# Performance work log

Measured on AMD Instinct MI355X. Metric: run time of the kernel, lower is better.

Reference implementation:

```python
import jax, jax.numpy as jnp
import numpy as np

N_NODES = 100_000
N_EDGES = 3_200_000
F_IN = 64
HID = 16
N_CLASSES = 4


def setup_inputs() -> dict:
    key = jax.random.key(0)
    ks = jax.random.split(key, 9)
    x = jax.random.normal(ks[0], (N_NODES, F_IN), dtype=jnp.float32)
    edge_index = jax.random.randint(ks[1], (2, N_EDGES), 0, N_NODES, dtype=jnp.int64)
    edge_weight = jax.random.uniform(ks[2], (N_EDGES,), dtype=jnp.float32)
    # Glorot-style init for the three GCN layer weights, zero bias (PyG default)
    W1 = jax.random.normal(ks[3], (F_IN, HID), dtype=jnp.float32) * (1.0 / np.sqrt(F_IN))
    b1 = jnp.zeros((HID,), jnp.float32)
    W3 = jax.random.normal(ks[4], (HID, HID), dtype=jnp.float32) * (1.0 / np.sqrt(HID))
    b3 = jnp.zeros((HID,), jnp.float32)
    W2 = jax.random.normal(ks[5], (HID, N_CLASSES), dtype=jnp.float32) * (1.0 / np.sqrt(HID))
    b2 = jnp.zeros((N_CLASSES,), jnp.float32)
    return {"x": x, "edge_index": edge_index, "edge_weight": edge_weight,
            "W1": W1, "b1": b1, "W3": W3, "b3": b3, "W2": W2, "b2": b2}


def reference(x, edge_index, edge_weight, W1, b1, W3, b3, W2, b2):
    n = x.shape[0]
    # GCNConv default: add self-loops with weight 1, symmetric deg^-1/2 norm
    loop = jnp.arange(n, dtype=edge_index.dtype)
    row = jnp.concatenate([edge_index[0], loop])  # source nodes
    col = jnp.concatenate([edge_index[1], loop])  # target nodes
    ew = jnp.concatenate([edge_weight, jnp.ones((n,), edge_weight.dtype)])
    deg = jax.ops.segment_sum(ew, col, num_segments=n)
    dinv = jnp.where(deg > 0, jax.lax.rsqrt(deg), 0.0)
    norm = dinv[row] * ew * dinv[col]  # [E+N]

    def gcn_conv(h, W, b):
        h = h @ W                                  # [N, out] small matmul first
        msg = norm[:, None] * h[row]               # gather + scale, [E+N, out]
        return jax.ops.segment_sum(msg, col, num_segments=n) + b

    h = jax.nn.relu(gcn_conv(x, W1, b1))
    # dropout is identity in eval mode (training=False)
    h = jax.nn.relu(gcn_conv(h, W3, b3))
    h = gcn_conv(h, W2, b2)
    return jax.nn.log_softmax(h, axis=1)
```

## Files before the change

### kernel.cpp

```cpp
#include <hip/hip_runtime.h>
#include <math.h>

#define NN 100000
#define NE 3200000
#define F_IN 64
#define HID 16
#define NC 4

#define SZB 200
#define NB 500
#define CAP 7424
#define CH 8192
#define NCH 391
#define NW 16

typedef _Float16 half_t;
typedef _Float16 h4f __attribute__((ext_vector_type(4)));

__device__ __forceinline__ unsigned bdiv(unsigned c) {
    return (unsigned)(((unsigned long long)c * 167773ull) >> 25);
}

__device__ __forceinline__ float upw(int pk) {
    unsigned short us = (unsigned short)(pk & 0x7fff);
    half_t h;
    __builtin_memcpy(&h, &us, 2);
    return (float)h;
}

__global__ __launch_bounds__(1024) void k_bin(const int* __restrict__ row,
                                              const int* __restrict__ col,
                                              const float* __restrict__ ew,
                                              int* __restrict__ cursor,
                                              unsigned* __restrict__ bpk,
                                              unsigned char* __restrict__ bcl) {
    __shared__ int h[NB];
    __shared__ int lstart[NB];
    __shared__ int gbase[NB];
    __shared__ int wsum[16];
    __shared__ uint2 s2[CH];
    int tid = threadIdx.x;
    int lane = tid & 63, wv = tid >> 6;
    for (int i = tid; i < NB; i += 1024) h[i] = 0;
    __syncthreads();
    int e0 = blockIdx.x * CH;
    int e1 = min(e0 + CH, NE);
    int eCnt = e1 - e0;
    int4 c4s[2];
#pragma unroll
    for (int it = 0; it < 2; it++) {
        int i = e0 + tid * 4 + it * 4096;
        if (i < e1) {
            int4 c4 = *(const int4*)(col + i);
            c4s[it] = c4;
            atomicAdd(&h[bdiv(c4.x)], 1);
            atomicAdd(&h[bdiv(c4.y)], 1);
            atomicAdd(&h[bdiv(c4.z)], 1);
            atomicAdd(&h[bdiv(c4.w)], 1);
        }
    }
    __syncthreads();
    int c0 = (tid < NB) ? h[tid] : 0;
    int v = c0;
#pragma unroll
    for (int off = 1; off < 64; off <<= 1) {
        int t = __shfl_up(v, off, 64);
        if (lane >= off) v += t;
    }
    if (lane == 63) wsum[wv] = v;
    __syncthreads();
    if (tid < NB) {
        int pre = 0;
#pragma unroll
        for (int ww = 0; ww < 8; ww++) pre += (ww < wv) ? wsum[ww] : 0;
        int ex = (v + pre) - c0;
        lstart[tid] = ex;
        h[tid] = ex;
        if (c0) gbase[tid] = tid * CAP + atomicAdd(&cursor[tid], c0);
    }
    __syncthreads();
#pragma unroll
    for (int it = 0; it < 2; it++) {
        int i = e0 + tid * 4 + it * 4096;
        if (i < e1) {
            int4 c4 = c4s[it];
            int4 r4 = *(const int4*)(row + i);
            float4 w4 = *(const float4*)(ew + i);
            half_t hw0 = (half_t)w4.x, hw1 = (half_t)w4.y, hw2 = (half_t)w4.z, hw3 = (half_t)w4.w;
            unsigned short b0, b1, b2, b3;
            __builtin_memcpy(&b0, &hw0, 2); __builtin_memcpy(&b1, &hw1, 2);
            __builtin_memcpy(&b2, &hw2, 2); __builtin_memcpy(&b3, &hw3, 2);
            int p; unsigned bb;
            bb = bdiv(c4.x); p = atomicAdd(&h[bb], 1);
            s2[p] = make_uint2(((unsigned)r4.x << 15) | (b0 & 0x7fff),
                               (bb << 8) | (unsigned)(c4.x - 200u * bb));
            bb = bdiv(c4.y); p = atomicAdd(&h[bb], 1);
            s2[p] = make_uint2(((unsigned)r4.y << 15) | (b1 & 0x7fff),
                               (bb << 8) | (unsigned)(c4.y - 200u * bb));
            bb = bdiv(c4.z); p = atomicAdd(&h[bb], 1);
            s2[p] = make_uint2(((unsigned)r4.z << 15) | (b2 & 0x7fff),
                               (bb << 8) | (unsigned)(c4.z - 200u * bb));
            bb = bdiv(c4.w); p = atomicAdd(&h[bb], 1);
            s2[p] = make_uint2(((unsigned)r4.w << 15) | (b3 & 0x7fff),
                               (bb << 8) | (unsigned)(c4.w - 200u * bb));
        }
    }
    __syncthreads();
    for (int i = tid; i < eCnt; i += 1024) {
        uint2 e2 = s2[i];
        int lo = (int)(e2.y >> 8);
        int d = gbase[lo] + (i - lstart[lo]);
        if (d < (lo + 1) * CAP) {
            bpk[d] = e2.x;
            bcl[d] = (unsigned char)(e2.y & 255u);
        }
    }
}

__global__ __launch_bounds__(1024) void k_sort(const unsigned* __restrict__ bpk,
                                               const unsigned char* __restrict__ bcl,
                                               const int* __restrict__ cursor,
                                               const float* __restrict__ x,
                                               const float* __restrict__ W1,
                                               unsigned* __restrict__ epk,
                                               int2* __restrict__ nodeptr2,
                                               float* __restrict__ dinv,
                                               half_t* __restrict__ tt1,
                                               int* __restrict__ perm) {
    __shared__ int hw[NW][SZB];
    __shared__ int cnt[SZB];
    __shared__ int ps[SZB];
    __shared__ int wsum4[4];
    __shared__ int h2[64];
    __shared__ int h2b[64];
    __shared__ unsigned stage[CAP];
    __shared__ float Ws[F_IN * HID];
    int b = blockIdx.x, tid = threadIdx.x;
    int lane = tid & 63;
    int w = tid >> 6;
    for (int i = tid; i < NW * SZB; i += 1024) ((int*)hw)[i] = 0;
    for (int i = tid; i < F_IN * HID; i += 1024) Ws[i] = W1[i];
    if (tid < 64) h2[tid] = 0;
    __syncthreads();
    int s = b * CAP;
    int m = min(cursor[b], CAP);
    int e = s + m;
    for (int i = s + tid; i < e; i += 1024)
        atomicAdd(&hw[w][bcl[i]], 1);
    __syncthreads();
    if (tid < SZB) {
        int c = 0;
#pragma unroll
        for (int ww = 0; ww < NW; ww++) c += hw[ww][tid];
        cnt[tid] = c;
    }
    __syncthreads();
    int pc = (tid < SZB) ? ((cnt[tid] + 3) & ~3) : 0;
    int key = 0;
    if (tid < SZB) {
        key = min(pc >> 2, 63);
        atomicAdd(&h2[key], 1);
    }
    int v = pc;
#pragma unroll
    for (int off = 1; off < 64; off <<= 1) {
        int t = __shfl_up(v, off, 64);
        if (lane >= off) v += t;
    }
    if (w < 4 && lane == 63) wsum4[w] = v;
    __syncthreads();
    if (tid < SZB) {
        int pre = 0;
#pragma unroll
        for (int ww = 0; ww < 4; ww++) pre += (ww < w) ? wsum4[ww] : 0;
        ps[tid] = v + pre;
    }
    if (tid < 64) {
        int c2 = h2[tid];
        int v2 = c2;
#pragma unroll
        for (int off = 1; off < 64; off <<= 1) {
            int t = __shfl_up(v2, off, 64);
            if (lane >= off) v2 += t;
        }
        h2b[tid] = v2 - c2;
    }
    __syncthreads();
    if (tid < SZB) {
        int rk = atomicAdd(&h2b[key], 1);
        perm[b * SZB + rk] = b * SZB + tid;
    }
    if (tid < SZB) {
        int run = ps[tid] - pc;
#pragma unroll
        for (int ww = 0; ww < NW; ww++) {
            int t = hw[ww][tid];
            hw[ww][tid] = run;
            run += t;
        }
    }
    __syncthreads();
    int mpad = min(ps[SZB - 1], CAP);
    for (int i = tid; i < mpad; i += 1024) stage[i] = 0u;
    __syncthreads();
    for (int i = s + tid; i < e; i += 1024) {
        int cl = bcl[i];
        int pos = atomicAdd(&hw[w][cl], 1);
        if (pos < CAP) stage[pos] = bpk[i];
    }
    __syncthreads();
    for (int i = tid; i < mpad; i += 1024) epk[s + i] = stage[i];
    int nl = tid >> 2, l = tid & 3;
    float di = 0.0f;
    int n = b * SZB + nl;
    if (nl < SZB) {
        int pcn = (cnt[nl] + 3) & ~3;
        int ex = ps[nl] - pcn;
        float sw = 0.0f;
        for (int i = ex + l; i < ex + pcn; i += 4) sw += upw((int)stage[i]);
        sw += __shfl_xor(sw, 1, 4);
        sw += __shfl_xor(sw, 2, 4);
        di = rsqrtf(1.0f + sw);
        if (n < NN && l == 0) {
            nodeptr2[n] = make_int2(s + ex, s + ex + pcn);
            dinv[n] = di;
        }
    }
    if (nl < SZB && n < NN) {
        float part[HID];
#pragma unroll
        for (int j = 0; j < HID; j++) part[j] = 0.0f;
        const float4* xp = (const float4*)(x + (size_t)n * F_IN) + l * 4;
#pragma unroll
        for (int k4 = 0; k4 < 4; k4++) {
            float4 vx = xp[k4];
            int k = l * 16 + k4 * 4;
#pragma unroll
            for (int j = 0; j < HID; j++) {
                part[j] += vx.x * Ws[(k + 0) * HID + j];
                part[j] += vx.y * Ws[(k + 1) * HID + j];
                part[j] += vx.z * Ws[(k + 2) * HID + j];
                part[j] += vx.w * Ws[(k + 3) * HID + j];
            }
        }
#pragma unroll
        for (int j = 0; j < HID; j++) {
            part[j] += __shfl_xor(part[j], 1, 4);
            part[j] += __shfl_xor(part[j], 2, 4);
        }
        h4f o;
        o.x = (half_t)(di * part[4 * l + 0]);
        o.y = (half_t)(di * part[4 * l + 1]);
        o.z = (half_t)(di * part[4 * l + 2]);
        o.w = (half_t)(di * part[4 * l + 3]);
        ((h4f*)tt1)[n * 4 + l] = o;
    }
}

#define ACC4(Q, V0, V1, V2, V3)                                                 \
    do {                                                                        \
        float w0 = upw((Q).x), w1 = upw((Q).y), w2 = upw((Q).z), w3 = upw((Q).w); \
        ax += w0 * (float)(V0).x; ay += w0 * (float)(V0).y;                     \
        az += w0 * (float)(V0).z; aw += w0 * (float)(V0).w;                     \
        ax += w1 * (float)(V1).x; ay += w1 * (float)(V1).y;                     \
        az += w1 * (float)(V1).z; aw += w1 * (float)(V1).w;                     \
        ax += w2 * (float)(V2).x; ay += w2 * (float)(V2).y;                     \
        az += w2 * (float)(V2).z; aw += w2 * (float)(V2).w;                     \
        ax += w3 * (float)(V3).x; ay += w3 * (float)(V3).y;                     \
        az += w3 * (float)(V3).z; aw += w3 * (float)(V3).w;                     \
    } while (0)

template <int DN>
__global__ __launch_bounds__(256) void k_aggf(const unsigned* __restrict__ epk,
                                              const int2* __restrict__ nptr,
                                              const int* __restrict__ perm,
                                              const half_t* __restrict__ tt_in,
                                              const float* __restrict__ bias,
                                              const float* __restrict__ dinv,
                                              const float* __restrict__ Wn,
                                              half_t* __restrict__ tt_out) {
    __shared__ float Ws[HID * DN];
    if (threadIdx.x < HID * DN) Ws[threadIdx.x] = Wn[threadIdx.x];
    __syncthreads();
    int tid = blockIdx.x * 256 + threadIdx.x;
    int g = tid >> 2;
    int l = tid & 3;
    if (g >= NN) return;
    int n = perm[g];
    int2 p = nptr[n];
    const h4f* ttp = (const h4f*)tt_in;
    h4f sv = ttp[n * 4 + l];
    float ax = 0.f, ay = 0.f, az = 0.f, aw = 0.f;
    int base = p.x;
    const int pend = p.y;
    if (base < pend) {
        int4 q = *(const int4*)(epk + base);
        base += 4;
        bool more = base < pend;
        int4 qn = *(const int4*)(epk + (more ? base : p.x));
        h4f v0 = ttp[((((unsigned)q.x) >> 15) << 2) + l];
        h4f v1 = ttp[((((unsigned)q.y) >> 15) << 2) + l];
        h4f v2 = ttp[((((unsigned)q.z) >> 15) << 2) + l];
        h4f v3 = ttp[((((unsigned)q.w) >> 15) << 2) + l];
        while (more) {
            base += 4;
            bool more2 = base < pend;
            int4 qnn = *(const int4*)(epk + (more2 ? base : p.x));
            h4f u0 = ttp[((((unsigned)qn.x) >> 15) << 2) + l];
            h4f u1 = ttp[((((unsigned)qn.y) >> 15) << 2) + l];
            h4f u2 = ttp[((((unsigned)qn.z) >> 15) << 2) + l];
            h4f u3 = ttp[((((unsigned)qn.w) >> 15) << 2) + l];
            ACC4(q, v0, v1, v2, v3);
            q = qn; qn = qnn;
            v0 = u0; v1 = u1; v2 = u2; v3 = u3;
            more = more2;
        }
        ACC4(q, v0, v1, v2, v3);
    }
    float di = dinv[n];
    const float4* b4p = (const float4*)bias;
    float4 b4 = b4p[l];
    float hreg[4];
    hreg[0] = fmaxf(b4.x + di * (ax + (float)sv.x), 0.f);
    hreg[1] = fmaxf(b4.y + di * (ay + (float)sv.y), 0.f);
    hreg[2] = fmaxf(b4.z + di * (az + (float)sv.z), 0.f);
    hreg[3] = fmaxf(b4.w + di * (aw + (float)sv.w), 0.f);
    if (DN == 16) {
        float ox = 0.f, oy = 0.f, oz = 0.f, ow = 0.f;
#pragma unroll
        for (int k = 0; k < HID; k++) {
            float hk = __shfl(hreg[k & 3], k >> 2, 4);
            const float4 wk = *(const float4*)&Ws[k * 16 + 4 * l];
            ox += hk * wk.x; oy += hk * wk.y; oz += hk * wk.z; ow += hk * wk.w;
        }
        h4f ov;
        ov.x = (half_t)(di * ox); ov.y = (half_t)(di * oy);
        ov.z = (half_t)(di * oz); ov.w = (half_t)(di * ow);
        ((h4f*)tt_out)[n * 4 + l] = ov;
    } else {
        float o = 0.f;
#pragma unroll
        for (int k = 0; k < HID; k++) {
            float hk = __shfl(hreg[k & 3], k >> 2, 4);
            o += hk * Ws[k * DN + l];
        }
        tt_out[(size_t)n * DN + l] = (half_t)(di * o);
    }
}

__global__ __launch_bounds__(256) void k_agg4sm(const unsigned* __restrict__ epk,
                                                const int2* __restrict__ nptr,
                                                const int* __restrict__ perm,
                                                const half_t* __restrict__ tt,
                                                const float* __restrict__ bias,
                                                const float* __restrict__ dinv,
                                                float* __restrict__ out) {
    int tid = blockIdx.x * 256 + threadIdx.x;
    int g = tid >> 2;
    int l = tid & 3;
    if (g >= NN) return;
    int n = perm[g];
    int2 p = nptr[n];
    float self = (float)tt[n * 4 + l];
    float acc = 0.f;
    int base = p.x;
    const int pend = p.y;
    if (base < pend) {
        int4 q = *(const int4*)(epk + base);
        base += 4;
        bool more = base < pend;
        int4 qn = *(const int4*)(epk + (more ? base : p.x));
        float v0 = (float)tt[((((unsigned)q.x) >> 15) << 2) + l];
        float v1 = (float)tt[((((unsigned)q.y) >> 15) << 2) + l];
        float v2 = (float)tt[((((unsigned)q.z) >> 15) << 2) + l];
        float v3 = (float)tt[((((unsigned)q.w) >> 15) << 2) + l];
        while (more) {
            base += 4;
            bool more2 = base < pend;
            int4 qnn = *(const int4*)(epk + (more2 ? base : p.x));
            float u0 = (float)tt[((((unsigned)qn.x) >> 15) << 2) + l];
            float u1 = (float)tt[((((unsigned)qn.y) >> 15) << 2) + l];
            float u2 = (float)tt[((((unsigned)qn.z) >> 15) << 2) + l];
            float u3 = (float)tt[((((unsigned)qn.w) >> 15) << 2) + l];
            acc += upw(q.x) * v0;
            acc += upw(q.y) * v1;
            acc += upw(q.z) * v2;
            acc += upw(q.w) * v3;
            q = qn; qn = qnn;
            v0 = u0; v1 = u1; v2 = u2; v3 = u3;
            more = more2;
        }
        acc += upw(q.x) * v0;
        acc += upw(q.y) * v1;
        acc += upw(q.z) * v2;
        acc += upw(q.w) * v3;
    }
    float di = dinv[n];
    float logit = bias[l] + di * (acc + self);
    float mx = logit;
    mx = fmaxf(mx, __shfl_xor(mx, 1, 4));
    mx = fmaxf(mx, __shfl_xor(mx, 2, 4));
    float ex = expf(logit - mx);
    float sm = ex;
    sm += __shfl_xor(sm, 1, 4);
    sm += __shfl_xor(sm, 2, 4);
    out[n * 4 + l] = logit - mx - logf(sm);
}

extern "C" void kernel_launch(void* const* d_in, const int* in_sizes, int n_in,
                              void* d_out, int out_size, void* d_ws, size_t ws_size,
                              hipStream_t stream) {
    const float* x  = (const float*)d_in[0];
    const int*   ei = (const int*)d_in[1];
    const float* ew = (const float*)d_in[2];
    const float* W1 = (const float*)d_in[3];
    const float* b1 = (const float*)d_in[4];
    const float* W3 = (const float*)d_in[5];
    const float* b3 = (const float*)d_in[6];
    const float* W2 = (const float*)d_in[7];
    const float* b2 = (const float*)d_in[8];
    float* out = (float*)d_out;

    const int* row = ei;
    const int* col = ei + NE;

    const size_t NEP = (size_t)NB * CAP;
    char* ws = (char*)d_ws;
    size_t off = 0;
    float*         dinv     = (float*)(ws + off);         off += 400000;
    int2*          nodeptr2 = (int2*)(ws + off);          off += 800000;
    int*           cursor   = (int*)(ws + off);           off += 2048;
    int*           perm     = (int*)(ws + off);           off += 400000;
    unsigned*      epk      = (unsigned*)(ws + off);      off += NEP * 4;
    unsigned*      bpk      = (unsigned*)(ws + off);      off += NEP * 4;
    unsigned char* bcl      = (unsigned char*)(ws + off); off += (NEP + 15) & ~15ull;
    half_t*        tt1      = (half_t*)(ws + off);        off += (size_t)NN * HID * 2;
    half_t*        tt2      = (half_t*)(ws + off);        off += (size_t)NN * HID * 2;
    half_t*        tt3      = (half_t*)(ws + off);        off += (size_t)NN * NC * 2;

    hipMemsetAsync(cursor, 0, NB * sizeof(int), stream);

    k_bin<<<NCH, 1024, 0, stream>>>(row, col, ew, cursor, bpk, bcl);
    k_sort<<<NB, 1024, 0, stream>>>(bpk, bcl, cursor, x, W1, epk, nodeptr2, dinv, tt1, perm);

    int gA = (NN * 4 + 255) / 256;

    k_aggf<HID><<<gA, 256, 0, stream>>>(epk, nodeptr2, perm, tt1, b1, dinv, W3, tt2);
    k_aggf<NC><<<gA, 256, 0, stream>>>(epk, nodeptr2, perm, tt2, b3, dinv, W2, tt3);
    k_agg4sm<<<gA, 256, 0, stream>>>(epk, nodeptr2, perm, tt3, b2, dinv, out);
}
```

Measured before the change: 223.7 us.

## Split each node's edge list across two lane groups and drop degree permutation

Aggregation kernels now assign 8 threads per node, each half processing half of the node's 4-edge chunks, then combine partial sums with a cross-lane shuffle; only one half writes output. The degree-bucketed node permutation built in the sort kernel is removed, so nodes are processed in natural order. This aims to double memory-level parallelism for the gather and remove the perm indirection and its construction, at the cost of more threads, redundant epilogue work, and possible load imbalance without degree sorting.

```diff
diff --git a/kernel.cpp b/kernel.cpp
--- a/kernel.cpp
+++ b/kernel.cpp
@@ -125,14 +125,11 @@
                                                unsigned* __restrict__ epk,
                                                int2* __restrict__ nodeptr2,
                                                float* __restrict__ dinv,
-                                               half_t* __restrict__ tt1,
-                                               int* __restrict__ perm) {
+                                               half_t* __restrict__ tt1) {
     __shared__ int hw[NW][SZB];
     __shared__ int cnt[SZB];
     __shared__ int ps[SZB];
     __shared__ int wsum4[4];
-    __shared__ int h2[64];
-    __shared__ int h2b[64];
     __shared__ unsigned stage[CAP];
     __shared__ float Ws[F_IN * HID];
     int b = blockIdx.x, tid = threadIdx.x;
@@ -140,7 +137,6 @@
     int w = tid >> 6;
     for (int i = tid; i < NW * SZB; i += 1024) ((int*)hw)[i] = 0;
     for (int i = tid; i < F_IN * HID; i += 1024) Ws[i] = W1[i];
-    if (tid < 64) h2[tid] = 0;
     __syncthreads();
     int s = b * CAP;
     int m = min(cursor[b], CAP);
@@ -156,11 +152,6 @@
     }
     __syncthreads();
     int pc = (tid < SZB) ? ((cnt[tid] + 3) & ~3) : 0;
-    int key = 0;
-    if (tid < SZB) {
-        key = min(pc >> 2, 63);
-        atomicAdd(&h2[key], 1);
-    }
     int v = pc;
 #pragma unroll
     for (int off = 1; off < 64; off <<= 1) {
@@ -175,21 +166,7 @@
         for (int ww = 0; ww < 4; ww++) pre += (ww < w) ? wsum4[ww] : 0;
         ps[tid] = v + pre;
     }
-    if (tid < 64) {
-        int c2 = h2[tid];
-        int v2 = c2;
-#pragma unroll
-        for (int off = 1; off < 64; off <<= 1) {
-            int t = __shfl_up(v2, off, 64);
-            if (lane >= off) v2 += t;
-        }
-        h2b[tid] = v2 - c2;
-    }
-    __syncthreads();
-    if (tid < SZB) {
-        int rk = atomicAdd(&h2b[key], 1);
-        perm[b * SZB + rk] = b * SZB + tid;
-    }
+    __syncthreads();
     if (tid < SZB) {
         int run = ps[tid] - pc;
 #pragma unroll
@@ -270,10 +247,16 @@
         az += w3 * (float)(V3).z; aw += w3 * (float)(V3).w;                     \
     } while (0)
 
+__device__ __forceinline__ void half_range(int px, int py, int h, int& b0, int& b1) {
+    int chunks = (py - px) >> 2;
+    int c0 = (chunks + 1) >> 1;
+    b0 = px + ((h == 0) ? 0 : c0 * 4);
+    b1 = (h == 0) ? (px + c0 * 4) : py;
+}
+
 template <int DN>
 __global__ __launch_bounds__(256) void k_aggf(const unsigned* __restrict__ epk,
                                               const int2* __restrict__ nptr,
-                                              const int* __restrict__ perm,
                                               const half_t* __restrict__ tt_in,
                                               const float* __restrict__ bias,
                                               const float* __restrict__ dinv,
@@ -283,16 +266,17 @@
     if (threadIdx.x < HID * DN) Ws[threadIdx.x] = Wn[threadIdx.x];
     __syncthreads();
     int tid = blockIdx.x * 256 + threadIdx.x;
-    int g = tid >> 2;
-    int l = tid & 3;
-    if (g >= NN) return;
-    int n = perm[g];
+    int n = tid >> 3;
+    int l = (tid >> 1) & 3;
+    l = tid & 3;
+    int h = (tid >> 2) & 1;
+    if (n >= NN) return;
     int2 p = nptr[n];
     const h4f* ttp = (const h4f*)tt_in;
     h4f sv = ttp[n * 4 + l];
     float ax = 0.f, ay = 0.f, az = 0.f, aw = 0.f;
-    int base = p.x;
-    const int pend = p.y;
+    int base, pend;
+    half_range(p.x, p.y, h, base, pend);
     if (base < pend) {
         int4 q = *(const int4*)(epk + base);
         base += 4;
@@ -317,6 +301,10 @@
         }
         ACC4(q, v0, v1, v2, v3);
     }
+    ax += __shfl_xor(ax, 4, 8);
+    ay += __shfl_xor(ay, 4, 8);
+    az += __shfl_xor(az, 4, 8);
+    aw += __shfl_xor(aw, 4, 8);
     float di = dinv[n];
     const float4* b4p = (const float4*)bias;
     float4 b4 = b4p[l];
@@ -333,10 +321,12 @@
             const float4 wk = *(const float4*)&Ws[k * 16 + 4 * l];
             ox += hk * wk.x; oy += hk * wk.y; oz += hk * wk.z; ow += hk * wk.w;
         }
-        h4f ov;
-        ov.x = (half_t)(di * ox); ov.y = (half_t)(di * oy);
-        ov.z = (half_t)(di * oz); ov.w = (half_t)(di * ow);
-        ((h4f*)tt_out)[n * 4 + l] = ov;
+        if (h == 0) {
+            h4f ov;
+            ov.x = (half_t)(di * ox); ov.y = (half_t)(di * oy);
+            ov.z = (half_t)(di * oz); ov.w = (half_t)(di * ow);
+            ((h4f*)tt_out)[n * 4 + l] = ov;
+        }
     } else {
         float o = 0.f;
 #pragma unroll
@@ -344,27 +334,26 @@
             float hk = __shfl(hreg[k & 3], k >> 2, 4);
             o += hk * Ws[k * DN + l];
         }
-        tt_out[(size_t)n * DN + l] = (half_t)(di * o);
+        if (h == 0) tt_out[(size_t)n * DN + l] = (half_t)(di * o);
     }
 }
 
 __global__ __launch_bounds__(256) void k_agg4sm(const unsigned* __restrict__ epk,
                                                 const int2* __restrict__ nptr,
-                                                const int* __restrict__ perm,
                                                 const half_t* __restrict__ tt,
                                                 const float* __restrict__ bias,
                                                 const float* __restrict__ dinv,
                                                 float* __restrict__ out) {
     int tid = blockIdx.x * 256 + threadIdx.x;
-    int g = tid >> 2;
+    int n = tid >> 3;
     int l = tid & 3;
-    if (g >= NN) return;
-    int n = perm[g];
+    int h = (tid >> 2) & 1;
+    if (n >= NN) return;
     int2 p = nptr[n];
     float self = (float)tt[n * 4 + l];
     float acc = 0.f;
-    int base = p.x;
-    const int pend = p.y;
+    int base, pend;
+    half_range(p.x, p.y, h, base, pend);
     if (base < pend) {
         int4 q = *(const int4*)(epk + base);
         base += 4;
@@ -395,6 +384,7 @@
         acc += upw(q.z) * v2;
         acc += upw(q.w) * v3;
     }
+    acc += __shfl_xor(acc, 4, 8);
     float di = dinv[n];
     float logit = bias[l] + di * (acc + self);
     float mx = logit;
@@ -404,7 +394,7 @@
     float sm = ex;
     sm += __shfl_xor(sm, 1, 4);
     sm += __shfl_xor(sm, 2, 4);
-    out[n * 4 + l] = logit - mx - logf(sm);
+    if (h == 0) out[n * 4 + l] = logit - mx - logf(sm);
 }
 
 extern "C" void kernel_launch(void* const* d_in, const int* in_sizes, int n_in,
@@ -430,7 +420,6 @@
     float*         dinv     = (float*)(ws + off);         off += 400000;
     int2*          nodeptr2 = (int2*)(ws + off);          off += 800000;
     int*           cursor   = (int*)(ws + off);           off += 2048;
-    int*           perm     = (int*)(ws + off);           off += 400000;
     unsigned*      epk      = (unsigned*)(ws + off);      off += NEP * 4;
     unsigned*      bpk      = (unsigned*)(ws + off);      off += NEP * 4;
     unsigned char* bcl      = (unsigned char*)(ws + off); off += (NEP + 15) & ~15ull;
@@ -441,11 +430,11 @@
     hipMemsetAsync(cursor, 0, NB * sizeof(int), stream);
 
     k_bin<<<NCH, 1024, 0, stream>>>(row, col, ew, cursor, bpk, bcl);
-    k_sort<<<NB, 1024, 0, stream>>>(bpk, bcl, cursor, x, W1, epk, nodeptr2, dinv, tt1, perm);
-
-    int gA = (NN * 4 + 255) / 256;
-
-    k_aggf<HID><<<gA, 256, 0, stream>>>(epk, nodeptr2, perm, tt1, b1, dinv, W3, tt2);
-    k_aggf<NC><<<gA, 256, 0, stream>>>(epk, nodeptr2, perm, tt2, b3, dinv, W2, tt3);
-    k_agg4sm<<<gA, 256, 0, stream>>>(epk, nodeptr2, perm, tt3, b2, dinv, out);
-}
+    k_sort<<<NB, 1024, 0, stream>>>(bpk, bcl, cursor, x, W1, epk, nodeptr2, dinv, tt1);
+
+    int gA8 = (NN * 8 + 255) / 256;
+
+    k_aggf<HID><<<gA8, 256, 0, stream>>>(epk, nodeptr2, tt1, b1, dinv, W3, tt2);
+    k_aggf<NC><<<gA8, 256, 0, stream>>>(epk, nodeptr2, tt2, b3, dinv, W2, tt3);
+    k_agg4sm<<<gA8, 256, 0, stream>>>(epk, nodeptr2, tt3, b2, dinv, out);
+}
```

New measurement: 210.5 us. 5.9% less time.
